# Performance work log

Hardware: AMD Instinct MI355X
Metric: run time of the kernel (lower is better)

Reference implementation:

```python
import jax, jax.numpy as jnp
import numpy as np

B, D, H = 1024, 64, 128


def setup_inputs() -> dict:
    key = jax.random.key(0)
    ks = jax.random.split(key, 12)
    s1 = 1.0 / np.sqrt(4 * D)
    sh = 1.0 / np.sqrt(H)
    sd = 1.0 / np.sqrt(D)
    return {
        "x": jax.random.normal(ks[0], (B, D), dtype=jnp.float32),
        # edge_fn: Linear(4D,H) -> ReLU -> Linear(H,H)
        "W1": jax.random.uniform(ks[1], (4 * D, H), minval=-s1, maxval=s1, dtype=jnp.float32),
        "b1": jax.random.uniform(ks[2], (H,), minval=-s1, maxval=s1, dtype=jnp.float32),
        "W2": jax.random.uniform(ks[3], (H, H), minval=-sh, maxval=sh, dtype=jnp.float32),
        "b2": jax.random.uniform(ks[4], (H,), minval=-sh, maxval=sh, dtype=jnp.float32),
        # tau_proj: Linear(D,1) -> Softplus
        "Wt": jax.random.uniform(ks[5], (D, 1), minval=-sd, maxval=sd, dtype=jnp.float32),
        "bt": jax.random.uniform(ks[6], (1,), minval=-sd, maxval=sd, dtype=jnp.float32),
        # agg: Linear(H,H) -> ReLU
        "Wa": jax.random.uniform(ks[7], (H, H), minval=-sh, maxval=sh, dtype=jnp.float32),
        "ba": jax.random.uniform(ks[8], (H,), minval=-sh, maxval=sh, dtype=jnp.float32),
        # res_proj: Linear(D,H)
        "Wr": jax.random.uniform(ks[9], (D, H), minval=-sd, maxval=sd, dtype=jnp.float32),
        "br": jax.random.uniform(ks[10], (H,), minval=-sd, maxval=sd, dtype=jnp.float32),
        # LayerNorm(H)
        "gamma": jnp.ones((H,), dtype=jnp.float32),
        "beta": jnp.zeros((H,), dtype=jnp.float32),
    }


def reference(x, W1, b1, W2, b2, Wt, bt, Wa, ba, Wr, br, gamma, beta):
    d = x.shape[1]
    # Decompose first linear over concat([x_i, x_j, delta, |delta|]) into 4 sub-matmuls;
    # only the |delta| term needs the pairwise [B,B,D] tensor.
    Wi, Wj, Wd, Wab = W1[:d], W1[d:2 * d], W1[2 * d:3 * d], W1[3 * d:]
    ti = x @ Wi            # [B,H] (i-dependent)
    tj = x @ Wj            # [B,H] (j-dependent)
    td = x @ Wd            # [B,H] (delta = x_i - x_j contribution)
    delta = x[:, None, :] - x[None, :, :]             # [B,B,D]
    ta = jnp.einsum('ijd,dh->ijh', jnp.abs(delta), Wab)  # [B,B,H]
    pre = ti[:, None, :] + tj[None, :, :] + td[:, None, :] - td[None, :, :] + ta + b1
    d_proj = jax.nn.relu(pre) @ W2 + b2               # [B,B,H]
    tau = jnp.maximum(jax.nn.softplus(x @ Wt + bt), 0.01) + 1.0  # [B,1]
    h_mean = d_proj.mean(axis=1) / tau                # mean over j
    h = jax.nn.relu(h_mean @ Wa + ba)
    y = h + (x @ Wr + br)
    mu = y.mean(axis=-1, keepdims=True)
    var = ((y - mu) ** 2).mean(axis=-1, keepdims=True)  # biased, like torch LayerNorm
    return (y - mu) * jax.lax.rsqrt(var + 1e-5) * gamma + beta
```

## Files before the change

### kernel.cpp

```cpp
#include <hip/hip_runtime.h>
#include <hip/hip_bf16.h>
#include <math.h>

#define BB 1024
#define DD 64
#define HH 128

typedef _Float16 half8 __attribute__((ext_vector_type(8)));
typedef __fp16 fp16x2 __attribute__((ext_vector_type(2)));
typedef float floatx4 __attribute__((ext_vector_type(4)));

union H8 { fp16x2 p[4]; half8 v; };

__device__ __forceinline__ void async_cp16(const float* g, float* lds_wave_base) {
    __builtin_amdgcn_global_load_lds(
        (const __attribute__((address_space(1))) unsigned int*)g,
        (__attribute__((address_space(3))) unsigned int*)lds_wave_base,
        16, 0, 0);
}

__global__ __launch_bounds__(256) void prep_kernel(
    const float* __restrict__ x, const float* __restrict__ W1,
    const float* __restrict__ b1,
    float* __restrict__ c1, float* __restrict__ c2P,
    _Float16* __restrict__ wpack)
{
    __shared__ float xs[8][DD];
    const int t = threadIdx.x;
    const int i0 = blockIdx.x * 8;
    xs[t >> 6][t & 63] = x[i0 * DD + t];
    xs[4 + (t >> 6)][t & 63] = x[i0 * DD + 256 + t];
    __syncthreads();

    const int ii = t >> 5;
    const int h4 = t & 31;
    const int h = h4 * 4;
    const int i = i0 + ii;

    if (blockIdx.y == 0) {
        float4 a1 = {0.f, 0.f, 0.f, 0.f};
        #pragma unroll 4
        for (int k = 0; k < DD; k++) {
            float4 wi = *(const float4*)(W1 + k * HH + h);
            float4 wd = *(const float4*)(W1 + (2 * DD + k) * HH + h);
            float xv = xs[ii][k];
            a1.x = fmaf(xv, wi.x + wd.x, a1.x);
            a1.y = fmaf(xv, wi.y + wd.y, a1.y);
            a1.z = fmaf(xv, wi.z + wd.z, a1.z);
            a1.w = fmaf(xv, wi.w + wd.w, a1.w);
        }
        float4 b1v = *(const float4*)(b1 + h);
        float4 c1v = {a1.x + b1v.x, a1.y + b1v.y, a1.z + b1v.z, a1.w + b1v.w};
        *(float4*)(c1 + i * HH + h) = c1v;
    } else {
        float4 a2 = {0.f, 0.f, 0.f, 0.f};
        #pragma unroll 4
        for (int k = 0; k < DD; k++) {
            float4 wj = *(const float4*)(W1 + (DD + k) * HH + h);
            float4 wd = *(const float4*)(W1 + (2 * DD + k) * HH + h);
            float xv = xs[ii][k];
            a2.x = fmaf(xv, wj.x - wd.x, a2.x);
            a2.y = fmaf(xv, wj.y - wd.y, a2.y);
            a2.z = fmaf(xv, wj.z - wd.z, a2.z);
            a2.w = fmaf(xv, wj.w - wd.w, a2.w);
        }
        const int jl = i & 15;
        float* cb = c2P + (i >> 4) * 2048 + (h >> 6) * 1024 + ((h >> 4) & 3) * 256 + (jl & 3);
        const int p0 = (jl >> 2) * 16 + (h & 15);
        cb[(p0 + 0) * 4] = a2.x;
        cb[(p0 + 1) * 4] = a2.y;
        cb[(p0 + 2) * 4] = a2.z;
        cb[(p0 + 3) * 4] = a2.w;

        if (blockIdx.x < 32) {
            int f = blockIdx.x * 256 + t;
            int jj = f & 7;
            int l  = (f >> 3) & 63;
            int u  = f >> 9;
            int s  = u & 1, t4 = (u >> 1) & 3, hh = u >> 3;
            int k  = s * 32 + ((l >> 4) << 3) + jj;
            int hcol = hh * 64 + t4 * 16 + (l & 15);
            wpack[f] = (_Float16)W1[(3 * DD + k) * HH + hcol];
        }
    }
}

__global__ __launch_bounds__(256, 4) void pair_kernel(
    const float* __restrict__ x, const float* __restrict__ c1,
    const float* __restrict__ c2P, const _Float16* __restrict__ wpack,
    float* __restrict__ Sp)
{
    __shared__ __align__(16) float xs[2][1024];
    __shared__ __align__(16) float c2s[2][1024];

    const int t = threadIdx.x;
    const int wave = t >> 6;
    const int l = t & 63;
    const int quad = l >> 4, lm = l & 15;
    const int bid = blockIdx.x;
    const int ig = bid >> 3;
    const int hh = (bid >> 2) & 1;
    const int jq = bid & 3;
    const int i = ig * 4 + wave;
    const int j0base = jq * 256;
    const int sw = lm & 7;

    async_cp16(x + (j0base + (t >> 4)) * DD + (((t & 15) ^ ((t >> 4) & 7)) << 2),
               &xs[0][0] + wave * 256);
    async_cp16(c2P + (j0base >> 4) * 2048 + hh * 1024 + t * 4,
               &c2s[0][0] + wave * 256);

    float xi[16];
    {
        const float* xg = x + i * DD + quad * 8;
        *(float4*)(xi)      = *(const float4*)(xg);
        *(float4*)(xi + 4)  = *(const float4*)(xg + 4);
        *(float4*)(xi + 8)  = *(const float4*)(xg + 32);
        *(float4*)(xi + 12) = *(const float4*)(xg + 36);
    }
    float c1r[4];
    #pragma unroll
    for (int t4 = 0; t4 < 4; t4++)
        c1r[t4] = c1[i * HH + hh * 64 + t4 * 16 + lm];
    half8 wf[8];
    #pragma unroll
    for (int u = 0; u < 8; u++)
        wf[u] = *(const half8*)(wpack + ((hh * 8 + u) * 64 + l) * 8);

    float S[4] = {0.f, 0.f, 0.f, 0.f};

    for (int tile = 0; tile < 16; ++tile) {
        const int cur = tile & 1;
        __syncthreads();

        if (tile < 15) {
            const int jn = j0base + (tile + 1) * 16;
            async_cp16(x + (jn + (t >> 4)) * DD + (((t & 15) ^ ((t >> 4) & 7)) << 2),
                       &xs[cur ^ 1][0] + wave * 256);
            async_cp16(c2P + (jn >> 4) * 2048 + hh * 1024 + t * 4,
                       &c2s[cur ^ 1][0] + wave * 256);
        }

        floatx4 acc[4];
        #pragma unroll
        for (int t4 = 0; t4 < 4; t4++) {
            float4 c2v = *(const float4*)(&c2s[cur][t4 * 256 + l * 4]);
            acc[t4][0] = c2v.x + c1r[t4];
            acc[t4][1] = c2v.y + c1r[t4];
            acc[t4][2] = c2v.z + c1r[t4];
            acc[t4][3] = c2v.w + c1r[t4];
        }

        const float* xb = &xs[cur][lm * 64];
        float4 a0 = *(const float4*)(xb + (((quad * 2)     ^ sw) << 2));
        float4 a1 = *(const float4*)(xb + (((quad * 2 + 1) ^ sw) << 2));
        float4 a2 = *(const float4*)(xb + (((quad * 2 + 8) ^ sw) << 2));
        float4 a3 = *(const float4*)(xb + (((quad * 2 + 9) ^ sw) << 2));
        H8 af0, af1;
        af0.p[0] = __builtin_amdgcn_cvt_pkrtz(fabsf(xi[0] - a0.x),  fabsf(xi[1] - a0.y));
        af0.p[1] = __builtin_amdgcn_cvt_pkrtz(fabsf(xi[2] - a0.z),  fabsf(xi[3] - a0.w));
        af0.p[2] = __builtin_amdgcn_cvt_pkrtz(fabsf(xi[4] - a1.x),  fabsf(xi[5] - a1.y));
        af0.p[3] = __builtin_amdgcn_cvt_pkrtz(fabsf(xi[6] - a1.z),  fabsf(xi[7] - a1.w));
        af1.p[0] = __builtin_amdgcn_cvt_pkrtz(fabsf(xi[8] - a2.x),  fabsf(xi[9] - a2.y));
        af1.p[1] = __builtin_amdgcn_cvt_pkrtz(fabsf(xi[10] - a2.z), fabsf(xi[11] - a2.w));
        af1.p[2] = __builtin_amdgcn_cvt_pkrtz(fabsf(xi[12] - a3.x), fabsf(xi[13] - a3.y));
        af1.p[3] = __builtin_amdgcn_cvt_pkrtz(fabsf(xi[14] - a3.z), fabsf(xi[15] - a3.w));

        #pragma unroll
        for (int t4 = 0; t4 < 4; t4++) {
            acc[t4] = __builtin_amdgcn_mfma_f32_16x16x32_f16(af0.v, wf[t4 * 2 + 0], acc[t4], 0, 0, 0);
            acc[t4] = __builtin_amdgcn_mfma_f32_16x16x32_f16(af1.v, wf[t4 * 2 + 1], acc[t4], 0, 0, 0);
        }
        #pragma unroll
        for (int t4 = 0; t4 < 4; t4++) {
            S[t4] += fmaxf(acc[t4][0], 0.f);
            S[t4] += fmaxf(acc[t4][1], 0.f);
            S[t4] += fmaxf(acc[t4][2], 0.f);
            S[t4] += fmaxf(acc[t4][3], 0.f);
        }
    }

    #pragma unroll
    for (int t4 = 0; t4 < 4; t4++) {
        S[t4] += __shfl_xor(S[t4], 16, 64);
        S[t4] += __shfl_xor(S[t4], 32, 64);
    }
    if (quad == 0) {
        #pragma unroll
        for (int t4 = 0; t4 < 4; t4++)
            Sp[(jq * BB + i) * HH + hh * 64 + t4 * 16 + lm] = S[t4];
    }
}

__global__ __launch_bounds__(128) void finish_kernel(
    const float* __restrict__ Sp, const float* __restrict__ W2,
    const float* __restrict__ b2, const float* __restrict__ x,
    const float* __restrict__ Wt, const float* __restrict__ bt,
    const float* __restrict__ Wa, const float* __restrict__ ba,
    const float* __restrict__ Wr, const float* __restrict__ br,
    const float* __restrict__ gamma, const float* __restrict__ beta,
    float* __restrict__ out)
{
    __shared__ float Srow[2][HH];
    __shared__ float mrow[2][HH];
    __shared__ float xrowS[2][DD];
    __shared__ float taus[2];
    const int t = threadIdx.x;
    const int ii = t >> 6;
    const int l = t & 63;
    const int i0 = blockIdx.x * 2;
    const int i = i0 + ii;
    const int h = l * 2;

    {
        float2 s = {0.f, 0.f};
        #pragma unroll
        for (int q = 0; q < 4; q++) {
            float2 v = *(const float2*)(Sp + (q * BB + i) * HH + h);
            s.x += v.x; s.y += v.y;
        }
        const float inv = 1.0f / (float)BB;
        Srow[ii][h]     = s.x * inv;
        Srow[ii][h + 1] = s.y * inv;
    }
    float xv0 = x[i * DD + l];
    xrowS[ii][l] = xv0;

    {
        float p = xv0 * Wt[l];
        #pragma unroll
        for (int off = 32; off; off >>= 1) p += __shfl_xor(p, off, 64);
        if (l == 0) {
            float z = p + bt[0];
            float sp = (z > 20.f) ? z : log1pf(expf(z));
            taus[ii] = fmaxf(sp, 0.01f) + 1.0f;
        }
    }
    __syncthreads();

    float2 acc = *(const float2*)(b2 + h);
    #pragma unroll 8
    for (int k = 0; k < HH; k++) {
        float2 w = *(const float2*)(W2 + k * HH + h);
        float sv = Srow[ii][k];
        acc.x = fmaf(sv, w.x, acc.x); acc.y = fmaf(sv, w.y, acc.y);
    }
    const float itau = 1.0f / taus[ii];
    mrow[ii][h]     = acc.x * itau;
    mrow[ii][h + 1] = acc.y * itau;
    __syncthreads();

    float2 a2 = *(const float2*)(ba + h);
    #pragma unroll 8
    for (int k = 0; k < HH; k++) {
        float2 w = *(const float2*)(Wa + k * HH + h);
        float sv = mrow[ii][k];
        a2.x = fmaf(sv, w.x, a2.x); a2.y = fmaf(sv, w.y, a2.y);
    }
    float2 brv = *(const float2*)(br + h);
    float2 y = {fmaxf(a2.x, 0.f) + brv.x, fmaxf(a2.y, 0.f) + brv.y};
    #pragma unroll 8
    for (int d = 0; d < DD; d++) {
        float2 w = *(const float2*)(Wr + d * HH + h);
        float xv = xrowS[ii][d];
        y.x = fmaf(xv, w.x, y.x); y.y = fmaf(xv, w.y, y.y);
    }

    float p = y.x + y.y;
    #pragma unroll
    for (int off = 32; off; off >>= 1) p += __shfl_xor(p, off, 64);
    float mu = p * (1.0f / (float)HH);
    float2 dy = {y.x - mu, y.y - mu};
    float q = dy.x * dy.x + dy.y * dy.y;
    #pragma unroll
    for (int off = 32; off; off >>= 1) q += __shfl_xor(q, off, 64);
    float rs = rsqrtf(q * (1.0f / (float)HH) + 1e-5f);
    float2 gv = *(const float2*)(gamma + h);
    float2 bv = *(const float2*)(beta + h);
    float2 o = {dy.x * rs * gv.x + bv.x, dy.y * rs * gv.y + bv.y};
    *(float2*)(out + i * HH + h) = o;
}

extern "C" void kernel_launch(void* const* d_in, const int* in_sizes, int n_in,
                              void* d_out, int out_size, void* d_ws, size_t ws_size,
                              hipStream_t stream)
{
    const float* x     = (const float*)d_in[0];
    const float* W1    = (const float*)d_in[1];
    const float* b1    = (const float*)d_in[2];
    const float* W2    = (const float*)d_in[3];
    const float* b2    = (const float*)d_in[4];
    const float* Wt    = (const float*)d_in[5];
    const float* bt    = (const float*)d_in[6];
    const float* Wa    = (const float*)d_in[7];
    const float* ba    = (const float*)d_in[8];
    const float* Wr    = (const float*)d_in[9];
    const float* br    = (const float*)d_in[10];
    const float* gamma = (const float*)d_in[11];
    const float* beta  = (const float*)d_in[12];
    float* out = (float*)d_out;

    char* ws = (char*)d_ws;
    float*     c1    = (float*)(ws);
    float*     c2P   = (float*)(ws + (512 << 10));
    _Float16*  wpack = (_Float16*)(ws + (1024 << 10));
    float*     Sp    = (float*)(ws + (1056 << 10));

    prep_kernel<<<dim3(128, 2), 256, 0, stream>>>(x, W1, b1, c1, c2P, wpack);
    pair_kernel<<<2048, 256, 0, stream>>>(x, c1, c2P, wpack, Sp);
    finish_kernel<<<512, 128, 0, stream>>>(Sp, W2, b2, x, Wt, bt,
                                           Wa, ba, Wr, br, gamma, beta, out);
}
```

Measured before the change: 130.8 us.

## Compute both hidden halves per block to reuse pairwise abs-delta fragments

```diff
diff --git a/kernel.cpp b/kernel.cpp
--- a/kernel.cpp
+++ b/kernel.cpp
@@ -91,15 +91,14 @@
     float* __restrict__ Sp)
 {
     __shared__ __align__(16) float xs[2][1024];
-    __shared__ __align__(16) float c2s[2][1024];
+    __shared__ __align__(16) float c2s[2][2048];
 
     const int t = threadIdx.x;
     const int wave = t >> 6;
     const int l = t & 63;
     const int quad = l >> 4, lm = l & 15;
     const int bid = blockIdx.x;
-    const int ig = bid >> 3;
-    const int hh = (bid >> 2) & 1;
+    const int ig = bid >> 2;
     const int jq = bid & 3;
     const int i = ig * 4 + wave;
     const int j0base = jq * 256;
@@ -107,8 +106,10 @@
 
     async_cp16(x + (j0base + (t >> 4)) * DD + (((t & 15) ^ ((t >> 4) & 7)) << 2),
                &xs[0][0] + wave * 256);
-    async_cp16(c2P + (j0base >> 4) * 2048 + hh * 1024 + t * 4,
+    async_cp16(c2P + (j0base >> 4) * 2048 + t * 4,
                &c2s[0][0] + wave * 256);
+    async_cp16(c2P + (j0base >> 4) * 2048 + (t + 256) * 4,
+               &c2s[0][0] + 1024 + wave * 256);
 
     float xi[16];
     {
@@ -118,16 +119,16 @@
         *(float4*)(xi + 8)  = *(const float4*)(xg + 32);
         *(float4*)(xi + 12) = *(const float4*)(xg + 36);
     }
-    float c1r[4];
-    #pragma unroll
-    for (int t4 = 0; t4 < 4; t4++)
-        c1r[t4] = c1[i * HH + hh * 64 + t4 * 16 + lm];
-    half8 wf[8];
+    float c1r[8];
     #pragma unroll
     for (int u = 0; u < 8; u++)
-        wf[u] = *(const half8*)(wpack + ((hh * 8 + u) * 64 + l) * 8);
-
-    float S[4] = {0.f, 0.f, 0.f, 0.f};
+        c1r[u] = c1[i * HH + (u >> 2) * 64 + (u & 3) * 16 + lm];
+    half8 wf[16];
+    #pragma unroll
+    for (int u = 0; u < 16; u++)
+        wf[u] = *(const half8*)(wpack + (u * 64 + l) * 8);
+
+    float S[8] = {0.f, 0.f, 0.f, 0.f, 0.f, 0.f, 0.f, 0.f};
 
     for (int tile = 0; tile < 16; ++tile) {
         const int cur = tile & 1;
@@ -137,18 +138,10 @@
             const int jn = j0base + (tile + 1) * 16;
             async_cp16(x + (jn + (t >> 4)) * DD + (((t & 15) ^ ((t >> 4) & 7)) << 2),
                        &xs[cur ^ 1][0] + wave * 256);
-            async_cp16(c2P + (jn >> 4) * 2048 + hh * 1024 + t * 4,
+            async_cp16(c2P + (jn >> 4) * 2048 + t * 4,
                        &c2s[cur ^ 1][0] + wave * 256);
-        }
-
-        floatx4 acc[4];
-        #pragma unroll
-        for (int t4 = 0; t4 < 4; t4++) {
-            float4 c2v = *(const float4*)(&c2s[cur][t4 * 256 + l * 4]);
-            acc[t4][0] = c2v.x + c1r[t4];
-            acc[t4][1] = c2v.y + c1r[t4];
-            acc[t4][2] = c2v.z + c1r[t4];
-            acc[t4][3] = c2v.w + c1r[t4];
+            async_cp16(c2P + (jn >> 4) * 2048 + (t + 256) * 4,
+                       &c2s[cur ^ 1][0] + 1024 + wave * 256);
         }
 
         const float* xb = &xs[cur][lm * 64];
@@ -167,28 +160,40 @@
         af1.p[3] = __builtin_amdgcn_cvt_pkrtz(fabsf(xi[14] - a3.z), fabsf(xi[15] - a3.w));
 
         #pragma unroll
-        for (int t4 = 0; t4 < 4; t4++) {
-            acc[t4] = __builtin_amdgcn_mfma_f32_16x16x32_f16(af0.v, wf[t4 * 2 + 0], acc[t4], 0, 0, 0);
-            acc[t4] = __builtin_amdgcn_mfma_f32_16x16x32_f16(af1.v, wf[t4 * 2 + 1], acc[t4], 0, 0, 0);
-        }
-        #pragma unroll
-        for (int t4 = 0; t4 < 4; t4++) {
-            S[t4] += fmaxf(acc[t4][0], 0.f);
-            S[t4] += fmaxf(acc[t4][1], 0.f);
-            S[t4] += fmaxf(acc[t4][2], 0.f);
-            S[t4] += fmaxf(acc[t4][3], 0.f);
-        }
-    }
-
-    #pragma unroll
-    for (int t4 = 0; t4 < 4; t4++) {
-        S[t4] += __shfl_xor(S[t4], 16, 64);
-        S[t4] += __shfl_xor(S[t4], 32, 64);
+        for (int hh2 = 0; hh2 < 2; hh2++) {
+            floatx4 acc[4];
+            #pragma unroll
+            for (int t4 = 0; t4 < 4; t4++) {
+                float4 c2v = *(const float4*)(&c2s[cur][hh2 * 1024 + t4 * 256 + l * 4]);
+                acc[t4][0] = c2v.x + c1r[hh2 * 4 + t4];
+                acc[t4][1] = c2v.y + c1r[hh2 * 4 + t4];
+                acc[t4][2] = c2v.z + c1r[hh2 * 4 + t4];
+                acc[t4][3] = c2v.w + c1r[hh2 * 4 + t4];
+            }
+            #pragma unroll
+            for (int t4 = 0; t4 < 4; t4++) {
+                acc[t4] = __builtin_amdgcn_mfma_f32_16x16x32_f16(af0.v, wf[hh2 * 8 + t4 * 2 + 0], acc[t4], 0, 0, 0);
+                acc[t4] = __builtin_amdgcn_mfma_f32_16x16x32_f16(af1.v, wf[hh2 * 8 + t4 * 2 + 1], acc[t4], 0, 0, 0);
+            }
+            #pragma unroll
+            for (int t4 = 0; t4 < 4; t4++) {
+                S[hh2 * 4 + t4] += fmaxf(acc[t4][0], 0.f);
+                S[hh2 * 4 + t4] += fmaxf(acc[t4][1], 0.f);
+                S[hh2 * 4 + t4] += fmaxf(acc[t4][2], 0.f);
+                S[hh2 * 4 + t4] += fmaxf(acc[t4][3], 0.f);
+            }
+        }
+    }
+
+    #pragma unroll
+    for (int u = 0; u < 8; u++) {
+        S[u] += __shfl_xor(S[u], 16, 64);
+        S[u] += __shfl_xor(S[u], 32, 64);
     }
     if (quad == 0) {
         #pragma unroll
-        for (int t4 = 0; t4 < 4; t4++)
-            Sp[(jq * BB + i) * HH + hh * 64 + t4 * 16 + lm] = S[t4];
+        for (int u = 0; u < 8; u++)
+            Sp[(jq * BB + i) * HH + (u >> 2) * 64 + (u & 3) * 16 + lm] = S[u];
     }
 }
 
@@ -307,7 +312,7 @@
     float*     Sp    = (float*)(ws + (1056 << 10));
 
     prep_kernel<<<dim3(128, 2), 256, 0, stream>>>(x, W1, b1, c1, c2P, wpack);
-    pair_kernel<<<2048, 256, 0, stream>>>(x, c1, c2P, wpack, Sp);
+    pair_kernel<<<1024, 256, 0, stream>>>(x, c1, c2P, wpack, Sp);
     finish_kernel<<<512, 128, 0, stream>>>(Sp, W2, b2, x, Wt, bt,
                                            Wa, ba, Wr, br, gamma, beta, out);
 }
```

New measurement: 195.0 us. 49.1% more time.
